# Kernel tuning notes

Hardware: AMD Instinct MI355X
Metric: run time of the kernel (lower is better)

## Reference

```python
import jax, jax.numpy as jnp
import numpy as np

MAX_AGENTS = 64
IN_DIM = 256
HID_DIM = 512
OUT_DIM = 256
MAX_CHILDREN = 8
BATCH = 1024


def setup_inputs() -> dict:
    key = jax.random.key(0)
    k1, k2, k3, k4, k5 = jax.random.split(key, 5)
    W1 = jax.random.normal(k1, (MAX_AGENTS, IN_DIM, HID_DIM), dtype=jnp.float32) * 0.02
    b1 = jnp.zeros((MAX_AGENTS, HID_DIM), dtype=jnp.float32)
    W2 = jax.random.normal(k2, (MAX_AGENTS, HID_DIM, OUT_DIM), dtype=jnp.float32) * 0.02
    b2 = jnp.zeros((MAX_AGENTS, OUT_DIM), dtype=jnp.float32)
    router_weights = jax.random.normal(k3, (MAX_AGENTS, HID_DIM, MAX_CHILDREN), dtype=jnp.float32) * 0.01
    agent_indices = jax.random.randint(k4, (BATCH,), 0, MAX_AGENTS, dtype=jnp.int64 if jax.config.jax_enable_x64 else jnp.int32)
    x = jax.random.normal(k5, (BATCH, IN_DIM), dtype=jnp.float32)
    return {
        "x": x,
        "W1": W1,
        "b1": b1,
        "W2": W2,
        "b2": b2,
        "router_weights": router_weights,
        "agent_indices": agent_indices,
    }


def reference(x, W1, b1, W2, b2, router_weights, agent_indices):
    # Gather per-sample weights (same as torch advanced indexing W1[agent_indices])
    w1 = W1[agent_indices]           # [B, In, Hid]
    b1g = b1[agent_indices]          # [B, Hid]
    w2 = W2[agent_indices]           # [B, Hid, Out]
    b2g = b2[agent_indices]          # [B, Out]
    rw = router_weights[agent_indices]  # [B, Hid, C]

    # per-sample MLP: bmm with a singleton row -> einsum
    h = jax.nn.relu(jnp.einsum('bi,bih->bh', x, w1) + b1g)      # [B, Hid]
    out = jnp.einsum('bh,bho->bo', h, w2) + b2g                 # [B, Out]
    r_logits = jnp.einsum('bh,bhc->bc', h, rw)                  # [B, C]
    return (h, out, r_logits)
```

## Files before the change

kernel.cpp:

```cpp
#include <hip/hip_runtime.h>

#define IN_DIM   256
#define HID_DIM  512
#define OUT_DIM  256
#define N_CHILD  8
#define BATCH    1024

#define SB    16
#define XPAD  20
#define MAXCH 128

__device__ __forceinline__ int sort_chunk(const int* __restrict__ raw, const int c,
                                          int* s_cnt, int* s_info, int* s_wsum,
                                          int* s_sid)
{
    const int t = threadIdx.x;
    const int lane = t & 63, w = t >> 6;
    if (t < 64) s_cnt[t] = 0;
    if (t == 0) { s_info[2] = 0; s_info[3] = 0; }
    __syncthreads();
    if (raw[2 * t + 1] != 0 || raw[2 * (t + 256) + 1] != 0) s_info[3] = 1;
    __syncthreads();
    const int is32 = s_info[3];
    int myid[4];
    #pragma unroll
    for (int j = 0; j < 4; ++j) {
        const int i = t * 4 + j;
        const int v = (is32 ? raw[i] : raw[2 * i]) & 63;
        myid[j] = v;
        atomicAdd(&s_cnt[v], 1);
    }
    __syncthreads();
    if (t < 64) {
        const int ca  = s_cnt[t];
        const int nch = (ca + SB - 1) / SB;
        int sn = nch;
        #pragma unroll
        for (int d = 1; d < 64; d <<= 1) {
            const int v = __shfl_up(sn, d);
            if (lane >= d) sn += v;
        }
        const int chb = sn - nch;
        if (c >= chb && c < chb + nch) {
            s_info[0] = t;
            const int p = (c - chb) * SB;
            s_info[1] = p;
            s_info[2] = (ca - p < SB) ? (ca - p) : SB;
        }
    }
    __syncthreads();
    const int len = s_info[2];
    if (len == 0) return 0;
    const int a = s_info[0], p = s_info[1];
    int m = 0;
    #pragma unroll
    for (int j = 0; j < 4; ++j) if (myid[j] == a) ++m;
    int inc = m;
    #pragma unroll
    for (int d = 1; d < 64; d <<= 1) {
        const int v = __shfl_up(inc, d);
        if (lane >= d) inc += v;
    }
    if (lane == 63) s_wsum[w] = inc;
    __syncthreads();
    int base = inc - m;
    #pragma unroll
    for (int ww = 0; ww < 4; ++ww) if (ww < w) base += s_wsum[ww];
    #pragma unroll
    for (int j = 0; j < 4; ++j)
        if (myid[j] == a) {
            const int r = (base++) - p;
            if (r >= 0 && r < SB) s_sid[r] = t * 4 + j;
        }
    __syncthreads();
    if (t >= len && t < SB) s_sid[t] = s_sid[len - 1];
    __syncthreads();
    return len;
}

extern "C" __global__ __launch_bounds__(256)
void k1_mlp1(const float* __restrict__ x, const float* __restrict__ W1,
             const float* __restrict__ b1, const float* __restrict__ rw,
             const int* __restrict__ raw,
             float* __restrict__ h_out, float* __restrict__ r_part)
{
    __shared__ float xT[IN_DIM * XPAD];
    __shared__ float wS[64 * 64];
    __shared__ int s_cnt[64], s_info[4], s_wsum[4], s_sid[SB];

    const int chunk = blockIdx.x;
    const int t = threadIdx.x;
    const int len = sort_chunk(raw, chunk, s_cnt, s_info, s_wsum, s_sid);
    if (len == 0) return;
    const int a    = s_info[0];
    const int bcol = blockIdx.y * 64;

    const float* Wb = W1 + (size_t)a * IN_DIM * HID_DIM + bcol;
    const int sr  = t >> 4;
    const int sc4 = (t & 15) * 4;
    #define WLD(P,I) (*(const float4*)(Wb + (size_t)((P)*64 + sr + (I)*16) * HID_DIM + sc4))

    float4 wr0 = WLD(0,0), wr1 = WLD(0,1), wr2 = WLD(0,2), wr3 = WLD(0,3);

    #pragma unroll
    for (int s = 0; s < SB; ++s)
        xT[t * XPAD + s] = x[(size_t)s_sid[s] * IN_DIM + t];

    const int cg = t & 15;
    const int kq = (t >> 4) & 3;
    const int w  = t >> 6;
    const bool act = (w * 4) < len;

    float acc[16];
    #pragma unroll
    for (int i = 0; i < 16; ++i) acc[i] = 0.f;

    for (int p = 0; p < IN_DIM / 64; ++p) {
        __syncthreads();
        *(float4*)(&wS[(sr +  0) * 64 + sc4]) = wr0;
        *(float4*)(&wS[(sr + 16) * 64 + sc4]) = wr1;
        *(float4*)(&wS[(sr + 32) * 64 + sc4]) = wr2;
        *(float4*)(&wS[(sr + 48) * 64 + sc4]) = wr3;
        __syncthreads();
        if (p < 3) {
            wr0 = WLD(p+1,0); wr1 = WLD(p+1,1);
            wr2 = WLD(p+1,2); wr3 = WLD(p+1,3);
        }
        if (act) {
            #pragma unroll
            for (int i = 0; i < 16; ++i) {
                const int row = i * 4 + kq;
                const float4 wv = *(const float4*)(&wS[row * 64 + cg * 4]);
                const float4 xv = *(const float4*)(&xT[(p * 64 + row) * XPAD + w * 4]);
                const float wa[4] = {wv.x, wv.y, wv.z, wv.w};
                const float xa[4] = {xv.x, xv.y, xv.z, xv.w};
                #pragma unroll
                for (int c = 0; c < 4; ++c)
                    #pragma unroll
                    for (int s = 0; s < 4; ++s)
                        acc[c * 4 + s] = fmaf(wa[c], xa[s], acc[c * 4 + s]);
            }
        }
    }
    #undef WLD

    if (!act) return;
    #pragma unroll
    for (int i = 0; i < 16; ++i) {
        acc[i] += __shfl_xor(acc[i], 16);
        acc[i] += __shfl_xor(acc[i], 32);
    }
    if (kq != 0) return;

    const float4 bv = *(const float4*)(b1 + a * HID_DIM + bcol + cg * 4);
    const float ba[4] = {bv.x, bv.y, bv.z, bv.w};
    float hv[16];
    #pragma unroll
    for (int c = 0; c < 4; ++c)
        #pragma unroll
        for (int s = 0; s < 4; ++s)
            hv[c * 4 + s] = fmaxf(acc[c * 4 + s] + ba[c], 0.f);

    #pragma unroll
    for (int s = 0; s < 4; ++s) {
        float4 v = make_float4(hv[0 * 4 + s], hv[1 * 4 + s],
                               hv[2 * 4 + s], hv[3 * 4 + s]);
        *(float4*)(h_out + (size_t)s_sid[w * 4 + s] * HID_DIM + bcol + cg * 4) = v;
    }

    float rp[32];
    #pragma unroll
    for (int i = 0; i < 32; ++i) rp[i] = 0.f;
    const float* rwa = rw + (size_t)a * HID_DIM * N_CHILD
                          + (size_t)(bcol + cg * 4) * N_CHILD;
    #pragma unroll
    for (int j = 0; j < 4; ++j)
        #pragma unroll
        for (int ch = 0; ch < 8; ++ch) {
            const float rv = rwa[j * N_CHILD + ch];
            #pragma unroll
            for (int s = 0; s < 4; ++s)
                rp[s * 8 + ch] = fmaf(hv[j * 4 + s], rv, rp[s * 8 + ch]);
        }
    #pragma unroll
    for (int i = 0; i < 32; ++i) {
        rp[i] += __shfl_xor(rp[i], 1);
        rp[i] += __shfl_xor(rp[i], 2);
        rp[i] += __shfl_xor(rp[i], 4);
        rp[i] += __shfl_xor(rp[i], 8);
    }
    if (cg == 0) {
        float* rb = r_part + ((size_t)chunk * 8 + blockIdx.y) * 128 + w * 32;
        #pragma unroll
        for (int s4 = 0; s4 < 8; ++s4)
            *(float4*)(rb + s4 * 4) = make_float4(rp[s4*4+0], rp[s4*4+1],
                                                  rp[s4*4+2], rp[s4*4+3]);
    }
}

extern "C" __global__ __launch_bounds__(256)
void k2_mlp2(const float* __restrict__ h, const float* __restrict__ W2,
             const float* __restrict__ b2, const int* __restrict__ raw,
             const float* __restrict__ r_part,
             float* __restrict__ o_out, float* __restrict__ r_out)
{
    __shared__ float hT[64 * XPAD];
    __shared__ float wS[64 * 32];
    __shared__ int s_cnt[64], s_info[4], s_wsum[4], s_sid[SB];

    const int chunk = blockIdx.x;
    const int t = threadIdx.x;
    const int len = sort_chunk(raw, chunk, s_cnt, s_info, s_wsum, s_sid);
    if (len == 0) return;
    const int a    = s_info[0];
    const int bcol = blockIdx.y * 32;

    const float* Wb = W2 + (size_t)a * HID_DIM * OUT_DIM + bcol;
    const int r2   = t >> 3;
    const int c4   = (t & 7) * 4;
    const int hrow = t & 63;
    const int hsb  = (t >> 6) * 4;
    #define WLD2(P,I) (*(const float4*)(Wb + (size_t)((P)*64 + r2 + (I)*32) * OUT_DIM + c4))
    #define HLD(P,J)  (h[(size_t)s_sid[hsb + (J)] * HID_DIM + (P)*64 + hrow])

    float4 wr0 = WLD2(0,0), wr1 = WLD2(0,1);
    float  hr0 = HLD(0,0), hr1 = HLD(0,1), hr2 = HLD(0,2), hr3 = HLD(0,3);

    const int cg = t & 7;
    const int kq = (t >> 3) & 7;
    const int w  = t >> 6;
    const bool act = (w * 4) < len;

    float acc[16];
    #pragma unroll
    for (int i = 0; i < 16; ++i) acc[i] = 0.f;

    for (int p = 0; p < HID_DIM / 64; ++p) {
        __syncthreads();
        hT[hrow * XPAD + hsb + 0] = hr0;
        hT[hrow * XPAD + hsb + 1] = hr1;
        hT[hrow * XPAD + hsb + 2] = hr2;
        hT[hrow * XPAD + hsb + 3] = hr3;
        *(float4*)(&wS[(r2 +  0) * 32 + c4]) = wr0;
        *(float4*)(&wS[(r2 + 32) * 32 + c4]) = wr1;
        __syncthreads();
        if (p < 7) {
            wr0 = WLD2(p+1,0); wr1 = WLD2(p+1,1);
            hr0 = HLD(p+1,0);  hr1 = HLD(p+1,1);
            hr2 = HLD(p+1,2);  hr3 = HLD(p+1,3);
        }
        if (act) {
            #pragma unroll
            for (int i = 0; i < 8; ++i) {
                const int row = i * 8 + kq;
                const float4 wv = *(const float4*)(&wS[row * 32 + cg * 4]);
                const float4 xv = *(const float4*)(&hT[row * XPAD + w * 4]);
                const float wa[4] = {wv.x, wv.y, wv.z, wv.w};
                const float xa[4] = {xv.x, xv.y, xv.z, xv.w};
                #pragma unroll
                for (int c = 0; c < 4; ++c)
                    #pragma unroll
                    for (int s = 0; s < 4; ++s)
                        acc[c * 4 + s] = fmaf(wa[c], xa[s], acc[c * 4 + s]);
            }
        }
    }
    #undef WLD2
    #undef HLD

    #pragma unroll
    for (int i = 0; i < 16; ++i) {
        acc[i] += __shfl_xor(acc[i], 8);
        acc[i] += __shfl_xor(acc[i], 16);
        acc[i] += __shfl_xor(acc[i], 32);
    }
    if (act && kq == 0) {
        const float4 bv = *(const float4*)(b2 + a * OUT_DIM + bcol + cg * 4);
        #pragma unroll
        for (int s = 0; s < 4; ++s) {
            const int g = w * 4 + s;
            if (g < len) {
                float4 v = make_float4(acc[0 * 4 + s] + bv.x,
                                       acc[1 * 4 + s] + bv.y,
                                       acc[2 * 4 + s] + bv.z,
                                       acc[3 * 4 + s] + bv.w);
                *(float4*)(o_out + (size_t)s_sid[g] * OUT_DIM + bcol + cg * 4) = v;
            }
        }
    }
    if (blockIdx.y == 0 && t < 128) {
        const int s = t >> 3;
        if (s < len) {
            float sum = 0.f;
            #pragma unroll
            for (int yy = 0; yy < 8; ++yy)
                sum += r_part[((size_t)chunk * 8 + yy) * 128 + t];
            r_out[(size_t)s_sid[s] * N_CHILD + (t & 7)] = sum;
        }
    }
}

extern "C" void kernel_launch(void* const* d_in, const int* in_sizes, int n_in,
                              void* d_out, int out_size, void* d_ws, size_t ws_size,
                              hipStream_t stream) {
    const float* x  = (const float*)d_in[0];
    const float* W1 = (const float*)d_in[1];
    const float* b1 = (const float*)d_in[2];
    const float* W2 = (const float*)d_in[3];
    const float* b2 = (const float*)d_in[4];
    const float* rw = (const float*)d_in[5];
    const int* raw  = (const int*)d_in[6];

    float* r_part = (float*)d_ws;

    float* out   = (float*)d_out;
    float* h_out = out;
    float* o_out = h_out + (size_t)BATCH * HID_DIM;
    float* r_out = o_out + (size_t)BATCH * OUT_DIM;

    hipLaunchKernelGGL(k1_mlp1, dim3(MAXCH, 8), dim3(256), 0, stream,
                       x, W1, b1, rw, raw, h_out, r_part);
    hipLaunchKernelGGL(k2_mlp2, dim3(MAXCH, 8), dim3(256), 0, stream,
                       h_out, W2, b2, raw, r_part, o_out, r_out);
}
```

Measured before the change: 129.2 us.

## Fuse both MLP stages into one cooperative kernel with grid sync and swizzled LDS

Merges the two per-agent GEMM kernels into a single cooperative launch that does a grid-wide sync between the hidden-layer and output-layer phases, so the per-chunk agent sort and the second kernel launch happen only once. Each thread now computes 8 columns instead of 4, and the weight tile in shared memory uses an XOR swizzle to avoid bank conflicts. Stage 2 now runs on only 4 of the 8 y-blocks with 64-wide tiles, and a fifth y-block does the router reduction. A grid sync across 1024 blocks is required, and if the cooperative launch fails the code falls back to two launches.

Result: slower. 477.3 us (+269.5%).

```diff
diff --git a/kernel.cpp b/kernel.cpp
--- a/kernel.cpp
+++ b/kernel.cpp
@@ -1,4 +1,7 @@
 #include <hip/hip_runtime.h>
+#include <hip/hip_cooperative_groups.h>
+
+namespace cg = cooperative_groups;
 
 #define IN_DIM   256
 #define HID_DIM  512
@@ -78,224 +81,230 @@
     return len;
 }
 
-extern "C" __global__ __launch_bounds__(256)
-void k1_mlp1(const float* __restrict__ x, const float* __restrict__ W1,
-             const float* __restrict__ b1, const float* __restrict__ rw,
-             const int* __restrict__ raw,
-             float* __restrict__ h_out, float* __restrict__ r_part)
+extern "C" __global__ __launch_bounds__(256, 4)
+void fused(const float* __restrict__ x, const float* __restrict__ W1,
+           const float* __restrict__ b1, const float* __restrict__ W2,
+           const float* __restrict__ b2, const float* __restrict__ rw,
+           const int* __restrict__ raw, float* __restrict__ h_out,
+           float* __restrict__ r_part, float* __restrict__ o_out,
+           float* __restrict__ r_out, int mode)
 {
-    __shared__ float xT[IN_DIM * XPAD];
+    __shared__ float sm[IN_DIM * XPAD];
     __shared__ float wS[64 * 64];
     __shared__ int s_cnt[64], s_info[4], s_wsum[4], s_sid[SB];
 
-    const int chunk = blockIdx.x;
+    const int c = blockIdx.x;
     const int t = threadIdx.x;
-    const int len = sort_chunk(raw, chunk, s_cnt, s_info, s_wsum, s_sid);
-    if (len == 0) return;
-    const int a    = s_info[0];
-    const int bcol = blockIdx.y * 64;
-
-    const float* Wb = W1 + (size_t)a * IN_DIM * HID_DIM + bcol;
-    const int sr  = t >> 4;
-    const int sc4 = (t & 15) * 4;
-    #define WLD(P,I) (*(const float4*)(Wb + (size_t)((P)*64 + sr + (I)*16) * HID_DIM + sc4))
-
-    float4 wr0 = WLD(0,0), wr1 = WLD(0,1), wr2 = WLD(0,2), wr3 = WLD(0,3);
-
-    #pragma unroll
-    for (int s = 0; s < SB; ++s)
-        xT[t * XPAD + s] = x[(size_t)s_sid[s] * IN_DIM + t];
-
-    const int cg = t & 15;
-    const int kq = (t >> 4) & 3;
-    const int w  = t >> 6;
-    const bool act = (w * 4) < len;
-
-    float acc[16];
-    #pragma unroll
-    for (int i = 0; i < 16; ++i) acc[i] = 0.f;
-
-    for (int p = 0; p < IN_DIM / 64; ++p) {
-        __syncthreads();
-        *(float4*)(&wS[(sr +  0) * 64 + sc4]) = wr0;
-        *(float4*)(&wS[(sr + 16) * 64 + sc4]) = wr1;
-        *(float4*)(&wS[(sr + 32) * 64 + sc4]) = wr2;
-        *(float4*)(&wS[(sr + 48) * 64 + sc4]) = wr3;
-        __syncthreads();
-        if (p < 3) {
-            wr0 = WLD(p+1,0); wr1 = WLD(p+1,1);
-            wr2 = WLD(p+1,2); wr3 = WLD(p+1,3);
-        }
-        if (act) {
-            #pragma unroll
-            for (int i = 0; i < 16; ++i) {
-                const int row = i * 4 + kq;
-                const float4 wv = *(const float4*)(&wS[row * 64 + cg * 4]);
-                const float4 xv = *(const float4*)(&xT[(p * 64 + row) * XPAD + w * 4]);
-                const float wa[4] = {wv.x, wv.y, wv.z, wv.w};
-                const float xa[4] = {xv.x, xv.y, xv.z, xv.w};
-                #pragma unroll
-                for (int c = 0; c < 4; ++c)
-                    #pragma unroll
-                    for (int s = 0; s < 4; ++s)
-                        acc[c * 4 + s] = fmaf(wa[c], xa[s], acc[c * 4 + s]);
-            }
-        }
-    }
-    #undef WLD
-
-    if (!act) return;
-    #pragma unroll
-    for (int i = 0; i < 16; ++i) {
-        acc[i] += __shfl_xor(acc[i], 16);
-        acc[i] += __shfl_xor(acc[i], 32);
-    }
-    if (kq != 0) return;
-
-    const float4 bv = *(const float4*)(b1 + a * HID_DIM + bcol + cg * 4);
-    const float ba[4] = {bv.x, bv.y, bv.z, bv.w};
-    float hv[16];
-    #pragma unroll
-    for (int c = 0; c < 4; ++c)
-        #pragma unroll
-        for (int s = 0; s < 4; ++s)
-            hv[c * 4 + s] = fmaxf(acc[c * 4 + s] + ba[c], 0.f);
-
-    #pragma unroll
-    for (int s = 0; s < 4; ++s) {
-        float4 v = make_float4(hv[0 * 4 + s], hv[1 * 4 + s],
-                               hv[2 * 4 + s], hv[3 * 4 + s]);
-        *(float4*)(h_out + (size_t)s_sid[w * 4 + s] * HID_DIM + bcol + cg * 4) = v;
-    }
-
-    float rp[32];
-    #pragma unroll
-    for (int i = 0; i < 32; ++i) rp[i] = 0.f;
-    const float* rwa = rw + (size_t)a * HID_DIM * N_CHILD
-                          + (size_t)(bcol + cg * 4) * N_CHILD;
-    #pragma unroll
-    for (int j = 0; j < 4; ++j)
-        #pragma unroll
-        for (int ch = 0; ch < 8; ++ch) {
-            const float rv = rwa[j * N_CHILD + ch];
-            #pragma unroll
-            for (int s = 0; s < 4; ++s)
-                rp[s * 8 + ch] = fmaf(hv[j * 4 + s], rv, rp[s * 8 + ch]);
-        }
-    #pragma unroll
-    for (int i = 0; i < 32; ++i) {
-        rp[i] += __shfl_xor(rp[i], 1);
-        rp[i] += __shfl_xor(rp[i], 2);
-        rp[i] += __shfl_xor(rp[i], 4);
-        rp[i] += __shfl_xor(rp[i], 8);
-    }
-    if (cg == 0) {
-        float* rb = r_part + ((size_t)chunk * 8 + blockIdx.y) * 128 + w * 32;
-        #pragma unroll
-        for (int s4 = 0; s4 < 8; ++s4)
-            *(float4*)(rb + s4 * 4) = make_float4(rp[s4*4+0], rp[s4*4+1],
-                                                  rp[s4*4+2], rp[s4*4+3]);
-    }
-}
-
-extern "C" __global__ __launch_bounds__(256)
-void k2_mlp2(const float* __restrict__ h, const float* __restrict__ W2,
-             const float* __restrict__ b2, const int* __restrict__ raw,
-             const float* __restrict__ r_part,
-             float* __restrict__ o_out, float* __restrict__ r_out)
-{
-    __shared__ float hT[64 * XPAD];
-    __shared__ float wS[64 * 32];
-    __shared__ int s_cnt[64], s_info[4], s_wsum[4], s_sid[SB];
-
-    const int chunk = blockIdx.x;
-    const int t = threadIdx.x;
-    const int len = sort_chunk(raw, chunk, s_cnt, s_info, s_wsum, s_sid);
-    if (len == 0) return;
-    const int a    = s_info[0];
-    const int bcol = blockIdx.y * 32;
-
-    const float* Wb = W2 + (size_t)a * HID_DIM * OUT_DIM + bcol;
-    const int r2   = t >> 3;
-    const int c4   = (t & 7) * 4;
-    const int hrow = t & 63;
-    const int hsb  = (t >> 6) * 4;
-    #define WLD2(P,I) (*(const float4*)(Wb + (size_t)((P)*64 + r2 + (I)*32) * OUT_DIM + c4))
-    #define HLD(P,J)  (h[(size_t)s_sid[hsb + (J)] * HID_DIM + (P)*64 + hrow])
-
-    float4 wr0 = WLD2(0,0), wr1 = WLD2(0,1);
-    float  hr0 = HLD(0,0), hr1 = HLD(0,1), hr2 = HLD(0,2), hr3 = HLD(0,3);
+    const int len = sort_chunk(raw, c, s_cnt, s_info, s_wsum, s_sid);
+    const int a   = s_info[0];
 
     const int cg = t & 7;
     const int kq = (t >> 3) & 7;
     const int w  = t >> 6;
     const bool act = (w * 4) < len;
-
-    float acc[16];
-    #pragma unroll
-    for (int i = 0; i < 16; ++i) acc[i] = 0.f;
-
-    for (int p = 0; p < HID_DIM / 64; ++p) {
-        __syncthreads();
-        hT[hrow * XPAD + hsb + 0] = hr0;
-        hT[hrow * XPAD + hsb + 1] = hr1;
-        hT[hrow * XPAD + hsb + 2] = hr2;
-        hT[hrow * XPAD + hsb + 3] = hr3;
-        *(float4*)(&wS[(r2 +  0) * 32 + c4]) = wr0;
-        *(float4*)(&wS[(r2 + 32) * 32 + c4]) = wr1;
-        __syncthreads();
-        if (p < 7) {
-            wr0 = WLD2(p+1,0); wr1 = WLD2(p+1,1);
-            hr0 = HLD(p+1,0);  hr1 = HLD(p+1,1);
-            hr2 = HLD(p+1,2);  hr3 = HLD(p+1,3);
-        }
+    const int sr  = t >> 4;
+    const int gc4 = (t & 15) * 4;
+    const int slt = ((t & 15) ^ sr) * 4;
+
+    if (mode != 2 && len > 0) {
+        const int bcol = blockIdx.y * 64;
+        const float* Wb = W1 + (size_t)a * IN_DIM * HID_DIM + bcol;
+        #define WLD(P,I) (*(const float4*)(Wb + (size_t)((P)*64 + sr + (I)*16) * HID_DIM + gc4))
+
+        float4 wr0 = WLD(0,0), wr1 = WLD(0,1), wr2 = WLD(0,2), wr3 = WLD(0,3);
+
+        #pragma unroll
+        for (int s = 0; s < SB; ++s)
+            sm[t * XPAD + s] = x[(size_t)s_sid[s] * IN_DIM + t];
+
+        float acc[32];
+        #pragma unroll
+        for (int i = 0; i < 32; ++i) acc[i] = 0.f;
+
+        for (int p = 0; p < IN_DIM / 64; ++p) {
+            __syncthreads();
+            *(float4*)(&wS[(sr +  0) * 64 + slt]) = wr0;
+            *(float4*)(&wS[(sr + 16) * 64 + slt]) = wr1;
+            *(float4*)(&wS[(sr + 32) * 64 + slt]) = wr2;
+            *(float4*)(&wS[(sr + 48) * 64 + slt]) = wr3;
+            __syncthreads();
+            if (p < 3) {
+                wr0 = WLD(p+1,0); wr1 = WLD(p+1,1);
+                wr2 = WLD(p+1,2); wr3 = WLD(p+1,3);
+            }
+            if (act) {
+                #pragma unroll
+                for (int i = 0; i < 8; ++i) {
+                    const int row = i * 8 + kq;
+                    const int rs  = row & 15;
+                    const float4 wv0 = *(const float4*)(&wS[row * 64 + ((2*cg    ^ rs) * 4)]);
+                    const float4 wv1 = *(const float4*)(&wS[row * 64 + (((2*cg+1) ^ rs) * 4)]);
+                    const float4 xv  = *(const float4*)(&sm[(p * 64 + row) * XPAD + w * 4]);
+                    const float wa[8] = {wv0.x, wv0.y, wv0.z, wv0.w,
+                                         wv1.x, wv1.y, wv1.z, wv1.w};
+                    const float xa[4] = {xv.x, xv.y, xv.z, xv.w};
+                    #pragma unroll
+                    for (int cc = 0; cc < 8; ++cc)
+                        #pragma unroll
+                        for (int s = 0; s < 4; ++s)
+                            acc[cc * 4 + s] = fmaf(wa[cc], xa[s], acc[cc * 4 + s]);
+                }
+            }
+        }
+        #undef WLD
+
         if (act) {
             #pragma unroll
-            for (int i = 0; i < 8; ++i) {
-                const int row = i * 8 + kq;
-                const float4 wv = *(const float4*)(&wS[row * 32 + cg * 4]);
-                const float4 xv = *(const float4*)(&hT[row * XPAD + w * 4]);
-                const float wa[4] = {wv.x, wv.y, wv.z, wv.w};
-                const float xa[4] = {xv.x, xv.y, xv.z, xv.w};
-                #pragma unroll
-                for (int c = 0; c < 4; ++c)
+            for (int i = 0; i < 32; ++i) {
+                acc[i] += __shfl_xor(acc[i], 8);
+                acc[i] += __shfl_xor(acc[i], 16);
+                acc[i] += __shfl_xor(acc[i], 32);
+            }
+            if (kq == 0) {
+                const float4 bv0 = *(const float4*)(b1 + a * HID_DIM + bcol + cg * 8);
+                const float4 bv1 = *(const float4*)(b1 + a * HID_DIM + bcol + cg * 8 + 4);
+                const float ba[8] = {bv0.x, bv0.y, bv0.z, bv0.w,
+                                     bv1.x, bv1.y, bv1.z, bv1.w};
+                float hv[32];
+                #pragma unroll
+                for (int cc = 0; cc < 8; ++cc)
                     #pragma unroll
                     for (int s = 0; s < 4; ++s)
-                        acc[c * 4 + s] = fmaf(wa[c], xa[s], acc[c * 4 + s]);
-            }
-        }
-    }
-    #undef WLD2
-    #undef HLD
-
-    #pragma unroll
-    for (int i = 0; i < 16; ++i) {
-        acc[i] += __shfl_xor(acc[i], 8);
-        acc[i] += __shfl_xor(acc[i], 16);
-        acc[i] += __shfl_xor(acc[i], 32);
-    }
-    if (act && kq == 0) {
-        const float4 bv = *(const float4*)(b2 + a * OUT_DIM + bcol + cg * 4);
-        #pragma unroll
-        for (int s = 0; s < 4; ++s) {
-            const int g = w * 4 + s;
-            if (g < len) {
-                float4 v = make_float4(acc[0 * 4 + s] + bv.x,
-                                       acc[1 * 4 + s] + bv.y,
-                                       acc[2 * 4 + s] + bv.z,
-                                       acc[3 * 4 + s] + bv.w);
-                *(float4*)(o_out + (size_t)s_sid[g] * OUT_DIM + bcol + cg * 4) = v;
-            }
-        }
-    }
-    if (blockIdx.y == 0 && t < 128) {
-        const int s = t >> 3;
-        if (s < len) {
-            float sum = 0.f;
+                        hv[cc * 4 + s] = fmaxf(acc[cc * 4 + s] + ba[cc], 0.f);
+
+                #pragma unroll
+                for (int s = 0; s < 4; ++s) {
+                    float* hb = h_out + (size_t)s_sid[w * 4 + s] * HID_DIM + bcol + cg * 8;
+                    *(float4*)(hb)     = make_float4(hv[0*4+s], hv[1*4+s], hv[2*4+s], hv[3*4+s]);
+                    *(float4*)(hb + 4) = make_float4(hv[4*4+s], hv[5*4+s], hv[6*4+s], hv[7*4+s]);
+                }
+
+                float rp[32];
+                #pragma unroll
+                for (int i = 0; i < 32; ++i) rp[i] = 0.f;
+                const float* rwa = rw + (size_t)a * HID_DIM * N_CHILD
+                                      + (size_t)(bcol + cg * 8) * N_CHILD;
+                #pragma unroll
+                for (int j = 0; j < 8; ++j)
+                    #pragma unroll
+                    for (int ch = 0; ch < 8; ++ch) {
+                        const float rv = rwa[j * N_CHILD + ch];
+                        #pragma unroll
+                        for (int s = 0; s < 4; ++s)
+                            rp[s * 8 + ch] = fmaf(hv[j * 4 + s], rv, rp[s * 8 + ch]);
+                    }
+                #pragma unroll
+                for (int i = 0; i < 32; ++i) {
+                    rp[i] += __shfl_xor(rp[i], 1);
+                    rp[i] += __shfl_xor(rp[i], 2);
+                    rp[i] += __shfl_xor(rp[i], 4);
+                }
+                if (cg == 0) {
+                    float* rb = r_part + ((size_t)c * 8 + blockIdx.y) * 128 + w * 32;
+                    #pragma unroll
+                    for (int s4 = 0; s4 < 8; ++s4)
+                        *(float4*)(rb + s4 * 4) = make_float4(rp[s4*4+0], rp[s4*4+1],
+                                                              rp[s4*4+2], rp[s4*4+3]);
+                }
+            }
+        }
+    }
+
+    if (mode == 0) {
+        __threadfence();
+        cg::this_grid().sync();
+        __threadfence();
+    }
+
+    if (mode != 1 && len > 0) {
+        if (blockIdx.y < 4) {
+            const int bcol = blockIdx.y * 64;
+            const float* Wb = W2 + (size_t)a * HID_DIM * OUT_DIM + bcol;
+            const int hrow = t & 63;
+            const int hsb  = (t >> 6) * 4;
+            #define WLD2(P,I) (*(const float4*)(Wb + (size_t)((P)*64 + sr + (I)*16) * OUT_DIM + gc4))
+            #define HLD(P,J)  (h_out[(size_t)s_sid[hsb + (J)] * HID_DIM + (P)*64 + hrow])
+
+            float4 wr0 = WLD2(0,0), wr1 = WLD2(0,1), wr2 = WLD2(0,2), wr3 = WLD2(0,3);
+            float  hr0 = HLD(0,0),  hr1 = HLD(0,1),  hr2 = HLD(0,2),  hr3 = HLD(0,3);
+
+            float acc[32];
             #pragma unroll
-            for (int yy = 0; yy < 8; ++yy)
-                sum += r_part[((size_t)chunk * 8 + yy) * 128 + t];
-            r_out[(size_t)s_sid[s] * N_CHILD + (t & 7)] = sum;
+            for (int i = 0; i < 32; ++i) acc[i] = 0.f;
+
+            for (int p = 0; p < HID_DIM / 64; ++p) {
+                __syncthreads();
+                sm[hrow * XPAD + hsb + 0] = hr0;
+                sm[hrow * XPAD + hsb + 1] = hr1;
+                sm[hrow * XPAD + hsb + 2] = hr2;
+                sm[hrow * XPAD + hsb + 3] = hr3;
+                *(float4*)(&wS[(sr +  0) * 64 + slt]) = wr0;
+                *(float4*)(&wS[(sr + 16) * 64 + slt]) = wr1;
+                *(float4*)(&wS[(sr + 32) * 64 + slt]) = wr2;
+                *(float4*)(&wS[(sr + 48) * 64 + slt]) = wr3;
+                __syncthreads();
+                if (p < 7) {
+                    wr0 = WLD2(p+1,0); wr1 = WLD2(p+1,1);
+                    wr2 = WLD2(p+1,2); wr3 = WLD2(p+1,3);
+                    hr0 = HLD(p+1,0);  hr1 = HLD(p+1,1);
+                    hr2 = HLD(p+1,2);  hr3 = HLD(p+1,3);
+                }
+                if (act) {
+                    #pragma unroll
+                    for (int i = 0; i < 8; ++i) {
+                        const int row = i * 8 + kq;
+                        const int rs  = row & 15;
+                        const float4 wv0 = *(const float4*)(&wS[row * 64 + ((2*cg    ^ rs) * 4)]);
+                        const float4 wv1 = *(const float4*)(&wS[row * 64 + (((2*cg+1) ^ rs) * 4)]);
+                        const float4 xv  = *(const float4*)(&sm[row * XPAD + w * 4]);
+                        const float wa[8] = {wv0.x, wv0.y, wv0.z, wv0.w,
+                                             wv1.x, wv1.y, wv1.z, wv1.w};
+                        const float xa[4] = {xv.x, xv.y, xv.z, xv.w};
+                        #pragma unroll
+                        for (int cc = 0; cc < 8; ++cc)
+                            #pragma unroll
+                            for (int s = 0; s < 4; ++s)
+                                acc[cc * 4 + s] = fmaf(wa[cc], xa[s], acc[cc * 4 + s]);
+                    }
+                }
+            }
+            #undef WLD2
+            #undef HLD
+
+            if (act) {
+                #pragma unroll
+                for (int i = 0; i < 32; ++i) {
+                    acc[i] += __shfl_xor(acc[i], 8);
+                    acc[i] += __shfl_xor(acc[i], 16);
+                    acc[i] += __shfl_xor(acc[i], 32);
+                }
+                if (kq == 0) {
+                    const float4 bv0 = *(const float4*)(b2 + a * OUT_DIM + bcol + cg * 8);
+                    const float4 bv1 = *(const float4*)(b2 + a * OUT_DIM + bcol + cg * 8 + 4);
+                    #pragma unroll
+                    for (int s = 0; s < 4; ++s) {
+                        const int g = w * 4 + s;
+                        if (g < len) {
+                            float* op = o_out + (size_t)s_sid[g] * OUT_DIM + bcol + cg * 8;
+                            *(float4*)(op)     = make_float4(acc[0*4+s] + bv0.x, acc[1*4+s] + bv0.y,
+                                                             acc[2*4+s] + bv0.z, acc[3*4+s] + bv0.w);
+                            *(float4*)(op + 4) = make_float4(acc[4*4+s] + bv1.x, acc[5*4+s] + bv1.y,
+                                                             acc[6*4+s] + bv1.z, acc[7*4+s] + bv1.w);
+                        }
+                    }
+                }
+            }
+        } else if (blockIdx.y == 4) {
+            if (t < 128) {
+                const int s = t >> 3;
+                if (s < len) {
+                    float sum = 0.f;
+                    #pragma unroll
+                    for (int yy = 0; yy < 8; ++yy)
+                        sum += r_part[((size_t)c * 8 + yy) * 128 + t];
+                    r_out[(size_t)s_sid[s] * N_CHILD + (t & 7)] = sum;
+                }
+            }
         }
     }
 }
@@ -318,8 +327,19 @@
     float* o_out = h_out + (size_t)BATCH * HID_DIM;
     float* r_out = o_out + (size_t)BATCH * OUT_DIM;
 
-    hipLaunchKernelGGL(k1_mlp1, dim3(MAXCH, 8), dim3(256), 0, stream,
-                       x, W1, b1, rw, raw, h_out, r_part);
-    hipLaunchKernelGGL(k2_mlp2, dim3(MAXCH, 8), dim3(256), 0, stream,
-                       h_out, W2, b2, raw, r_part, o_out, r_out);
+    int mode = 0;
+    void* args[] = {(void*)&x, (void*)&W1, (void*)&b1, (void*)&W2, (void*)&b2,
+                    (void*)&rw, (void*)&raw, (void*)&h_out, (void*)&r_part,
+                    (void*)&o_out, (void*)&r_out, (void*)&mode};
+    hipError_t e = hipLaunchCooperativeKernel((const void*)fused, dim3(MAXCH, 8),
+                                              dim3(256), args, 0, stream);
+    if (e != hipSuccess) {
+        (void)hipGetLastError();
+        hipLaunchKernelGGL(fused, dim3(MAXCH, 8), dim3(256), 0, stream,
+                           x, W1, b1, W2, b2, rw, raw, h_out, r_part,
+                           o_out, r_out, 1);
+        hipLaunchKernelGGL(fused, dim3(MAXCH, 8), dim3(256), 0, stream,
+                           x, W1, b1, W2, b2, rw, raw, h_out, r_part,
+                           o_out, r_out, 2);
+    }
 }
```

## Read weights directly from global memory instead of staging through LDS tiles

Applied to the files above, without the earlier changes.

Both MLP kernels stop cooperatively staging weight tiles into shared memory with register double-buffering. Each thread now reads its float4 weight slice straight from global memory inside a fully unrolled k loop, relying on L1/L2 for the reuse across waves. This removes the per-tile barriers and the LDS traffic. k2 now stages h in two 256-row halves, and both kernels request 4 blocks per CU via launch bounds. The cost is that all four waves in a block read the same weight addresses redundantly from cache, and register pressure rises from the deep unroll.

New measurement: 145.1 us. +12.4%, slower.

```diff
diff --git a/kernel.cpp b/kernel.cpp
--- a/kernel.cpp
+++ b/kernel.cpp
@@ -78,73 +78,52 @@
     return len;
 }
 
-extern "C" __global__ __launch_bounds__(256)
+extern "C" __global__ __launch_bounds__(256, 4)
 void k1_mlp1(const float* __restrict__ x, const float* __restrict__ W1,
              const float* __restrict__ b1, const float* __restrict__ rw,
              const int* __restrict__ raw,
              float* __restrict__ h_out, float* __restrict__ r_part)
 {
     __shared__ float xT[IN_DIM * XPAD];
-    __shared__ float wS[64 * 64];
     __shared__ int s_cnt[64], s_info[4], s_wsum[4], s_sid[SB];
 
-    const int chunk = blockIdx.x;
+    const int c = blockIdx.x;
     const int t = threadIdx.x;
-    const int len = sort_chunk(raw, chunk, s_cnt, s_info, s_wsum, s_sid);
+    const int len = sort_chunk(raw, c, s_cnt, s_info, s_wsum, s_sid);
     if (len == 0) return;
-    const int a    = s_info[0];
+    const int a = s_info[0];
     const int bcol = blockIdx.y * 64;
-
-    const float* Wb = W1 + (size_t)a * IN_DIM * HID_DIM + bcol;
-    const int sr  = t >> 4;
-    const int sc4 = (t & 15) * 4;
-    #define WLD(P,I) (*(const float4*)(Wb + (size_t)((P)*64 + sr + (I)*16) * HID_DIM + sc4))
-
-    float4 wr0 = WLD(0,0), wr1 = WLD(0,1), wr2 = WLD(0,2), wr3 = WLD(0,3);
 
     #pragma unroll
     for (int s = 0; s < SB; ++s)
         xT[t * XPAD + s] = x[(size_t)s_sid[s] * IN_DIM + t];
+    __syncthreads();
 
     const int cg = t & 15;
     const int kq = (t >> 4) & 3;
     const int w  = t >> 6;
-    const bool act = (w * 4) < len;
+    if (w * 4 >= len) return;
+
+    const float* Wb = W1 + (size_t)a * IN_DIM * HID_DIM + bcol + cg * 4;
 
     float acc[16];
     #pragma unroll
     for (int i = 0; i < 16; ++i) acc[i] = 0.f;
 
-    for (int p = 0; p < IN_DIM / 64; ++p) {
-        __syncthreads();
-        *(float4*)(&wS[(sr +  0) * 64 + sc4]) = wr0;
-        *(float4*)(&wS[(sr + 16) * 64 + sc4]) = wr1;
-        *(float4*)(&wS[(sr + 32) * 64 + sc4]) = wr2;
-        *(float4*)(&wS[(sr + 48) * 64 + sc4]) = wr3;
-        __syncthreads();
-        if (p < 3) {
-            wr0 = WLD(p+1,0); wr1 = WLD(p+1,1);
-            wr2 = WLD(p+1,2); wr3 = WLD(p+1,3);
-        }
-        if (act) {
-            #pragma unroll
-            for (int i = 0; i < 16; ++i) {
-                const int row = i * 4 + kq;
-                const float4 wv = *(const float4*)(&wS[row * 64 + cg * 4]);
-                const float4 xv = *(const float4*)(&xT[(p * 64 + row) * XPAD + w * 4]);
-                const float wa[4] = {wv.x, wv.y, wv.z, wv.w};
-                const float xa[4] = {xv.x, xv.y, xv.z, xv.w};
-                #pragma unroll
-                for (int c = 0; c < 4; ++c)
-                    #pragma unroll
-                    for (int s = 0; s < 4; ++s)
-                        acc[c * 4 + s] = fmaf(wa[c], xa[s], acc[c * 4 + s]);
-            }
-        }
-    }
-    #undef WLD
-
-    if (!act) return;
+    #pragma unroll
+    for (int i = 0; i < 64; ++i) {
+        const int row = i * 4 + kq;
+        const float4 wv = *(const float4*)(Wb + (size_t)row * HID_DIM);
+        const float4 xv = *(const float4*)(&xT[row * XPAD + w * 4]);
+        const float wa[4] = {wv.x, wv.y, wv.z, wv.w};
+        const float xa[4] = {xv.x, xv.y, xv.z, xv.w};
+        #pragma unroll
+        for (int cc = 0; cc < 4; ++cc)
+            #pragma unroll
+            for (int s = 0; s < 4; ++s)
+                acc[cc * 4 + s] = fmaf(wa[cc], xa[s], acc[cc * 4 + s]);
+    }
+
     #pragma unroll
     for (int i = 0; i < 16; ++i) {
         acc[i] += __shfl_xor(acc[i], 16);
@@ -156,10 +135,10 @@
     const float ba[4] = {bv.x, bv.y, bv.z, bv.w};
     float hv[16];
     #pragma unroll
-    for (int c = 0; c < 4; ++c)
+    for (int cc = 0; cc < 4; ++cc)
         #pragma unroll
         for (int s = 0; s < 4; ++s)
-            hv[c * 4 + s] = fmaxf(acc[c * 4 + s] + ba[c], 0.f);
+            hv[cc * 4 + s] = fmaxf(acc[cc * 4 + s] + ba[cc], 0.f);
 
     #pragma unroll
     for (int s = 0; s < 4; ++s) {
@@ -190,7 +169,7 @@
         rp[i] += __shfl_xor(rp[i], 8);
     }
     if (cg == 0) {
-        float* rb = r_part + ((size_t)chunk * 8 + blockIdx.y) * 128 + w * 32;
+        float* rb = r_part + ((size_t)c * 8 + blockIdx.y) * 128 + w * 32;
         #pragma unroll
         for (int s4 = 0; s4 < 8; ++s4)
             *(float4*)(rb + s4 * 4) = make_float4(rp[s4*4+0], rp[s4*4+1],
@@ -198,93 +177,74 @@
     }
 }
 
-extern "C" __global__ __launch_bounds__(256)
+extern "C" __global__ __launch_bounds__(256, 4)
 void k2_mlp2(const float* __restrict__ h, const float* __restrict__ W2,
              const float* __restrict__ b2, const int* __restrict__ raw,
              const float* __restrict__ r_part,
              float* __restrict__ o_out, float* __restrict__ r_out)
 {
-    __shared__ float hT[64 * XPAD];
-    __shared__ float wS[64 * 32];
+    __shared__ float hT[256 * XPAD];
     __shared__ int s_cnt[64], s_info[4], s_wsum[4], s_sid[SB];
 
-    const int chunk = blockIdx.x;
+    const int c = blockIdx.x;
     const int t = threadIdx.x;
-    const int len = sort_chunk(raw, chunk, s_cnt, s_info, s_wsum, s_sid);
+    const int len = sort_chunk(raw, c, s_cnt, s_info, s_wsum, s_sid);
     if (len == 0) return;
-    const int a    = s_info[0];
+    const int a = s_info[0];
     const int bcol = blockIdx.y * 32;
-
-    const float* Wb = W2 + (size_t)a * HID_DIM * OUT_DIM + bcol;
-    const int r2   = t >> 3;
-    const int c4   = (t & 7) * 4;
-    const int hrow = t & 63;
-    const int hsb  = (t >> 6) * 4;
-    #define WLD2(P,I) (*(const float4*)(Wb + (size_t)((P)*64 + r2 + (I)*32) * OUT_DIM + c4))
-    #define HLD(P,J)  (h[(size_t)s_sid[hsb + (J)] * HID_DIM + (P)*64 + hrow])
-
-    float4 wr0 = WLD2(0,0), wr1 = WLD2(0,1);
-    float  hr0 = HLD(0,0), hr1 = HLD(0,1), hr2 = HLD(0,2), hr3 = HLD(0,3);
 
     const int cg = t & 7;
     const int kq = (t >> 3) & 7;
     const int w  = t >> 6;
     const bool act = (w * 4) < len;
+    const float* Wb = W2 + (size_t)a * HID_DIM * OUT_DIM + bcol + cg * 4;
 
     float acc[16];
     #pragma unroll
     for (int i = 0; i < 16; ++i) acc[i] = 0.f;
 
-    for (int p = 0; p < HID_DIM / 64; ++p) {
+    #pragma unroll
+    for (int half = 0; half < 2; ++half) {
+        const int kb = half * 256;
+        #pragma unroll
+        for (int s = 0; s < SB; ++s)
+            hT[t * XPAD + s] = h[(size_t)s_sid[s] * HID_DIM + kb + t];
         __syncthreads();
-        hT[hrow * XPAD + hsb + 0] = hr0;
-        hT[hrow * XPAD + hsb + 1] = hr1;
-        hT[hrow * XPAD + hsb + 2] = hr2;
-        hT[hrow * XPAD + hsb + 3] = hr3;
-        *(float4*)(&wS[(r2 +  0) * 32 + c4]) = wr0;
-        *(float4*)(&wS[(r2 + 32) * 32 + c4]) = wr1;
-        __syncthreads();
-        if (p < 7) {
-            wr0 = WLD2(p+1,0); wr1 = WLD2(p+1,1);
-            hr0 = HLD(p+1,0);  hr1 = HLD(p+1,1);
-            hr2 = HLD(p+1,2);  hr3 = HLD(p+1,3);
-        }
         if (act) {
             #pragma unroll
-            for (int i = 0; i < 8; ++i) {
+            for (int i = 0; i < 32; ++i) {
                 const int row = i * 8 + kq;
-                const float4 wv = *(const float4*)(&wS[row * 32 + cg * 4]);
+                const float4 wv = *(const float4*)(Wb + (size_t)(kb + row) * OUT_DIM);
                 const float4 xv = *(const float4*)(&hT[row * XPAD + w * 4]);
                 const float wa[4] = {wv.x, wv.y, wv.z, wv.w};
                 const float xa[4] = {xv.x, xv.y, xv.z, xv.w};
                 #pragma unroll
-                for (int c = 0; c < 4; ++c)
+                for (int cc = 0; cc < 4; ++cc)
                     #pragma unroll
                     for (int s = 0; s < 4; ++s)
-                        acc[c * 4 + s] = fmaf(wa[c], xa[s], acc[c * 4 + s]);
+                        acc[cc * 4 + s] = fmaf(wa[cc], xa[s], acc[cc * 4 + s]);
             }
         }
-    }
-    #undef WLD2
-    #undef HLD
-
-    #pragma unroll
-    for (int i = 0; i < 16; ++i) {
-        acc[i] += __shfl_xor(acc[i], 8);
-        acc[i] += __shfl_xor(acc[i], 16);
-        acc[i] += __shfl_xor(acc[i], 32);
-    }
-    if (act && kq == 0) {
-        const float4 bv = *(const float4*)(b2 + a * OUT_DIM + bcol + cg * 4);
-        #pragma unroll
-        for (int s = 0; s < 4; ++s) {
-            const int g = w * 4 + s;
-            if (g < len) {
-                float4 v = make_float4(acc[0 * 4 + s] + bv.x,
-                                       acc[1 * 4 + s] + bv.y,
-                                       acc[2 * 4 + s] + bv.z,
-                                       acc[3 * 4 + s] + bv.w);
-                *(float4*)(o_out + (size_t)s_sid[g] * OUT_DIM + bcol + cg * 4) = v;
+        if (half == 0) __syncthreads();
+    }
+
+    if (act) {
+        #pragma unroll
+        for (int i = 0; i < 16; ++i) {
+            acc[i] += __shfl_xor(acc[i], 8);
+            acc[i] += __shfl_xor(acc[i], 16);
+            acc[i] += __shfl_xor(acc[i], 32);
+        }
+        if (kq == 0) {
+            const float4 bv = *(const float4*)(b2 + a * OUT_DIM + bcol + cg * 4);
+            #pragma unroll
+            for (int s = 0; s < 4; ++s) {
+                const int g = w * 4 + s;
+                if (g < len) {
+                    float4 v = make_float4(acc[0*4+s] + bv.x, acc[1*4+s] + bv.y,
+                                           acc[2*4+s] + bv.z, acc[3*4+s] + bv.w);
+                    *(float4*)(o_out + (size_t)s_sid[g] * OUT_DIM + bcol + cg * 4) = v;
+                }
             }
         }
     }
@@ -294,7 +254,7 @@
             float sum = 0.f;
             #pragma unroll
             for (int yy = 0; yy < 8; ++yy)
-                sum += r_part[((size_t)chunk * 8 + yy) * 128 + t];
+                sum += r_part[((size_t)c * 8 + yy) * 128 + t];
             r_out[(size_t)s_sid[s] * N_CHILD + (t & 7)] = sum;
         }
     }
```

## Double per-block sample chunk and move router logits into second kernel

Applied to the files above, without the earlier changes.

Grows the per-agent chunk from 16 to 32 samples, so each weight tile is reused across twice as many samples and fewer chunks (96 max) are launched. The x tile is staged in two halves to keep shared memory small. The router logit computation moves from the first kernel's epilogue, which used partial sums and a workspace reduction, into the second kernel. There, blockIdx.y==0 blocks accumulate h·rw directly from the shared h tile. This removes the r_part round trip but doubles accumulator registers and adds serial router work to one column of blocks.

Measured after the change: 128.1 us. No clear change (-0.8%).

```diff
diff --git a/kernel.cpp b/kernel.cpp
--- a/kernel.cpp
+++ b/kernel.cpp
@@ -6,9 +6,9 @@
 #define N_CHILD  8
 #define BATCH    1024
 
-#define SB    16
-#define XPAD  20
-#define MAXCH 128
+#define SB    32
+#define XS    36
+#define MAXCH 96
 
 __device__ __forceinline__ int sort_chunk(const int* __restrict__ raw, const int c,
                                           int* s_cnt, int* s_info, int* s_wsum,
@@ -80,19 +80,18 @@
 
 extern "C" __global__ __launch_bounds__(256)
 void k1_mlp1(const float* __restrict__ x, const float* __restrict__ W1,
-             const float* __restrict__ b1, const float* __restrict__ rw,
-             const int* __restrict__ raw,
-             float* __restrict__ h_out, float* __restrict__ r_part)
+             const float* __restrict__ b1, const int* __restrict__ raw,
+             float* __restrict__ h_out)
 {
-    __shared__ float xT[IN_DIM * XPAD];
+    __shared__ float xT[128 * XS];
     __shared__ float wS[64 * 64];
     __shared__ int s_cnt[64], s_info[4], s_wsum[4], s_sid[SB];
 
-    const int chunk = blockIdx.x;
+    const int c = blockIdx.x;
     const int t = threadIdx.x;
-    const int len = sort_chunk(raw, chunk, s_cnt, s_info, s_wsum, s_sid);
+    const int len = sort_chunk(raw, c, s_cnt, s_info, s_wsum, s_sid);
     if (len == 0) return;
-    const int a    = s_info[0];
+    const int a = s_info[0];
     const int bcol = blockIdx.y * 64;
 
     const float* Wb = W1 + (size_t)a * IN_DIM * HID_DIM + bcol;
@@ -102,26 +101,39 @@
 
     float4 wr0 = WLD(0,0), wr1 = WLD(0,1), wr2 = WLD(0,2), wr3 = WLD(0,3);
 
-    #pragma unroll
-    for (int s = 0; s < SB; ++s)
-        xT[t * XPAD + s] = x[(size_t)s_sid[s] * IN_DIM + t];
+    const int xrow = t & 127;
+    const int xsg  = (t >> 7) * 16;
+    #pragma unroll
+    for (int j = 0; j < 16; ++j)
+        xT[xrow * XS + xsg + j] = x[(size_t)s_sid[xsg + j] * IN_DIM + xrow];
 
     const int cg = t & 15;
     const int kq = (t >> 4) & 3;
     const int w  = t >> 6;
-    const bool act = (w * 4) < len;
-
-    float acc[16];
-    #pragma unroll
-    for (int i = 0; i < 16; ++i) acc[i] = 0.f;
-
-    for (int p = 0; p < IN_DIM / 64; ++p) {
+    const bool act = (w * 8) < len;
+
+    float acc[32];
+    #pragma unroll
+    for (int i = 0; i < 32; ++i) acc[i] = 0.f;
+    float xh[16];
+
+    for (int p = 0; p < 4; ++p) {
         __syncthreads();
+        if (p == 2) {
+            #pragma unroll
+            for (int j = 0; j < 16; ++j)
+                xT[xrow * XS + xsg + j] = xh[j];
+        }
         *(float4*)(&wS[(sr +  0) * 64 + sc4]) = wr0;
         *(float4*)(&wS[(sr + 16) * 64 + sc4]) = wr1;
         *(float4*)(&wS[(sr + 32) * 64 + sc4]) = wr2;
         *(float4*)(&wS[(sr + 48) * 64 + sc4]) = wr3;
         __syncthreads();
+        if (p == 1) {
+            #pragma unroll
+            for (int j = 0; j < 16; ++j)
+                xh[j] = x[(size_t)s_sid[xsg + j] * IN_DIM + 128 + xrow];
+        }
         if (p < 3) {
             wr0 = WLD(p+1,0); wr1 = WLD(p+1,1);
             wr2 = WLD(p+1,2); wr3 = WLD(p+1,3);
@@ -130,15 +142,18 @@
             #pragma unroll
             for (int i = 0; i < 16; ++i) {
                 const int row = i * 4 + kq;
-                const float4 wv = *(const float4*)(&wS[row * 64 + cg * 4]);
-                const float4 xv = *(const float4*)(&xT[(p * 64 + row) * XPAD + w * 4]);
+                const int lr  = (p & 1) * 64 + row;
+                const float4 wv  = *(const float4*)(&wS[row * 64 + cg * 4]);
+                const float4 xv0 = *(const float4*)(&xT[lr * XS + w * 8]);
+                const float4 xv1 = *(const float4*)(&xT[lr * XS + w * 8 + 4]);
                 const float wa[4] = {wv.x, wv.y, wv.z, wv.w};
-                const float xa[4] = {xv.x, xv.y, xv.z, xv.w};
+                const float xa[8] = {xv0.x, xv0.y, xv0.z, xv0.w,
+                                     xv1.x, xv1.y, xv1.z, xv1.w};
                 #pragma unroll
-                for (int c = 0; c < 4; ++c)
+                for (int cc = 0; cc < 4; ++cc)
                     #pragma unroll
-                    for (int s = 0; s < 4; ++s)
-                        acc[c * 4 + s] = fmaf(wa[c], xa[s], acc[c * 4 + s]);
+                    for (int s = 0; s < 8; ++s)
+                        acc[cc * 8 + s] = fmaf(wa[cc], xa[s], acc[cc * 8 + s]);
             }
         }
     }
@@ -146,130 +161,120 @@
 
     if (!act) return;
     #pragma unroll
-    for (int i = 0; i < 16; ++i) {
+    for (int i = 0; i < 32; ++i) {
         acc[i] += __shfl_xor(acc[i], 16);
         acc[i] += __shfl_xor(acc[i], 32);
     }
     if (kq != 0) return;
 
     const float4 bv = *(const float4*)(b1 + a * HID_DIM + bcol + cg * 4);
-    const float ba[4] = {bv.x, bv.y, bv.z, bv.w};
-    float hv[16];
-    #pragma unroll
-    for (int c = 0; c < 4; ++c)
-        #pragma unroll
-        for (int s = 0; s < 4; ++s)
-            hv[c * 4 + s] = fmaxf(acc[c * 4 + s] + ba[c], 0.f);
-
-    #pragma unroll
-    for (int s = 0; s < 4; ++s) {
-        float4 v = make_float4(hv[0 * 4 + s], hv[1 * 4 + s],
-                               hv[2 * 4 + s], hv[3 * 4 + s]);
-        *(float4*)(h_out + (size_t)s_sid[w * 4 + s] * HID_DIM + bcol + cg * 4) = v;
-    }
-
-    float rp[32];
-    #pragma unroll
-    for (int i = 0; i < 32; ++i) rp[i] = 0.f;
-    const float* rwa = rw + (size_t)a * HID_DIM * N_CHILD
-                          + (size_t)(bcol + cg * 4) * N_CHILD;
-    #pragma unroll
-    for (int j = 0; j < 4; ++j)
-        #pragma unroll
-        for (int ch = 0; ch < 8; ++ch) {
-            const float rv = rwa[j * N_CHILD + ch];
-            #pragma unroll
-            for (int s = 0; s < 4; ++s)
-                rp[s * 8 + ch] = fmaf(hv[j * 4 + s], rv, rp[s * 8 + ch]);
-        }
-    #pragma unroll
-    for (int i = 0; i < 32; ++i) {
-        rp[i] += __shfl_xor(rp[i], 1);
-        rp[i] += __shfl_xor(rp[i], 2);
-        rp[i] += __shfl_xor(rp[i], 4);
-        rp[i] += __shfl_xor(rp[i], 8);
-    }
-    if (cg == 0) {
-        float* rb = r_part + ((size_t)chunk * 8 + blockIdx.y) * 128 + w * 32;
-        #pragma unroll
-        for (int s4 = 0; s4 < 8; ++s4)
-            *(float4*)(rb + s4 * 4) = make_float4(rp[s4*4+0], rp[s4*4+1],
-                                                  rp[s4*4+2], rp[s4*4+3]);
+    #pragma unroll
+    for (int s = 0; s < 8; ++s) {
+        float4 v = make_float4(fmaxf(acc[0*8+s] + bv.x, 0.f),
+                               fmaxf(acc[1*8+s] + bv.y, 0.f),
+                               fmaxf(acc[2*8+s] + bv.z, 0.f),
+                               fmaxf(acc[3*8+s] + bv.w, 0.f));
+        *(float4*)(h_out + (size_t)s_sid[w * 8 + s] * HID_DIM + bcol + cg * 4) = v;
     }
 }
 
 extern "C" __global__ __launch_bounds__(256)
 void k2_mlp2(const float* __restrict__ h, const float* __restrict__ W2,
-             const float* __restrict__ b2, const int* __restrict__ raw,
-             const float* __restrict__ r_part,
+             const float* __restrict__ b2, const float* __restrict__ rw,
+             const int* __restrict__ raw,
              float* __restrict__ o_out, float* __restrict__ r_out)
 {
-    __shared__ float hT[64 * XPAD];
+    __shared__ float hT[64 * XS];
     __shared__ float wS[64 * 32];
+    __shared__ float rwS[64 * N_CHILD];
     __shared__ int s_cnt[64], s_info[4], s_wsum[4], s_sid[SB];
 
-    const int chunk = blockIdx.x;
+    const int c = blockIdx.x;
     const int t = threadIdx.x;
-    const int len = sort_chunk(raw, chunk, s_cnt, s_info, s_wsum, s_sid);
+    const int len = sort_chunk(raw, c, s_cnt, s_info, s_wsum, s_sid);
     if (len == 0) return;
-    const int a    = s_info[0];
+    const int a = s_info[0];
     const int bcol = blockIdx.y * 32;
-
-    const float* Wb = W2 + (size_t)a * HID_DIM * OUT_DIM + bcol;
-    const int r2   = t >> 3;
+    const bool router = (blockIdx.y == 0);
+
+    const float* Wb  = W2 + (size_t)a * HID_DIM * OUT_DIM + bcol;
+    const float* rwp = rw + (size_t)a * HID_DIM * N_CHILD;
+    const int r2w  = t >> 3;
     const int c4   = (t & 7) * 4;
     const int hrow = t & 63;
-    const int hsb  = (t >> 6) * 4;
-    #define WLD2(P,I) (*(const float4*)(Wb + (size_t)((P)*64 + r2 + (I)*32) * OUT_DIM + c4))
-    #define HLD(P,J)  (h[(size_t)s_sid[hsb + (J)] * HID_DIM + (P)*64 + hrow])
-
-    float4 wr0 = WLD2(0,0), wr1 = WLD2(0,1);
-    float  hr0 = HLD(0,0), hr1 = HLD(0,1), hr2 = HLD(0,2), hr3 = HLD(0,3);
+    const int hsb  = (t >> 6) * 8;
+    #define WLD2(P,I) (*(const float4*)(Wb + (size_t)((P)*64 + r2w + (I)*32) * OUT_DIM + c4))
+
+    float4 wA0 = WLD2(0,0), wA1 = WLD2(0,1);
+    float hA[8], hB[8];
+    #pragma unroll
+    for (int j = 0; j < 8; ++j)
+        hA[j] = h[(size_t)s_sid[hsb + j] * HID_DIM + hrow];
+    float rA0 = 0.f, rA1 = 0.f;
+    if (router) { rA0 = rwp[t]; rA1 = rwp[256 + t]; }
 
     const int cg = t & 7;
     const int kq = (t >> 3) & 7;
     const int w  = t >> 6;
-    const bool act = (w * 4) < len;
-
-    float acc[16];
-    #pragma unroll
-    for (int i = 0; i < 16; ++i) acc[i] = 0.f;
-
-    for (int p = 0; p < HID_DIM / 64; ++p) {
+    const bool act = (w * 8) < len;
+    const int rs  = t >> 3;
+    const int rch = t & 7;
+
+    float acc[32];
+    #pragma unroll
+    for (int i = 0; i < 32; ++i) acc[i] = 0.f;
+    float racc = 0.f;
+
+    for (int p = 0; p < 8; ++p) {
         __syncthreads();
-        hT[hrow * XPAD + hsb + 0] = hr0;
-        hT[hrow * XPAD + hsb + 1] = hr1;
-        hT[hrow * XPAD + hsb + 2] = hr2;
-        hT[hrow * XPAD + hsb + 3] = hr3;
-        *(float4*)(&wS[(r2 +  0) * 32 + c4]) = wr0;
-        *(float4*)(&wS[(r2 + 32) * 32 + c4]) = wr1;
+        #pragma unroll
+        for (int j = 0; j < 8; ++j)
+            hT[hrow * XS + hsb + j] = hA[j];
+        *(float4*)(&wS[(r2w +  0) * 32 + c4]) = wA0;
+        *(float4*)(&wS[(r2w + 32) * 32 + c4]) = wA1;
+        if (router) { rwS[t] = rA0; rwS[256 + t] = rA1; }
         __syncthreads();
         if (p < 7) {
-            wr0 = WLD2(p+1,0); wr1 = WLD2(p+1,1);
-            hr0 = HLD(p+1,0);  hr1 = HLD(p+1,1);
-            hr2 = HLD(p+1,2);  hr3 = HLD(p+1,3);
+            wA0 = WLD2(p+1,0); wA1 = WLD2(p+1,1);
+            #pragma unroll
+            for (int j = 0; j < 8; ++j)
+                hB[j] = h[(size_t)s_sid[hsb + j] * HID_DIM + (p+1)*64 + hrow];
+            if (router) {
+                rA0 = rwp[(size_t)(p+1)*512 + t];
+                rA1 = rwp[(size_t)(p+1)*512 + 256 + t];
+            }
         }
         if (act) {
             #pragma unroll
             for (int i = 0; i < 8; ++i) {
                 const int row = i * 8 + kq;
-                const float4 wv = *(const float4*)(&wS[row * 32 + cg * 4]);
-                const float4 xv = *(const float4*)(&hT[row * XPAD + w * 4]);
+                const float4 wv  = *(const float4*)(&wS[row * 32 + cg * 4]);
+                const float4 xv0 = *(const float4*)(&hT[row * XS + w * 8]);
+                const float4 xv1 = *(const float4*)(&hT[row * XS + w * 8 + 4]);
                 const float wa[4] = {wv.x, wv.y, wv.z, wv.w};
-                const float xa[4] = {xv.x, xv.y, xv.z, xv.w};
+                const float xa[8] = {xv0.x, xv0.y, xv0.z, xv0.w,
+                                     xv1.x, xv1.y, xv1.z, xv1.w};
                 #pragma unroll
-                for (int c = 0; c < 4; ++c)
+                for (int cc = 0; cc < 4; ++cc)
                     #pragma unroll
-                    for (int s = 0; s < 4; ++s)
-                        acc[c * 4 + s] = fmaf(wa[c], xa[s], acc[c * 4 + s]);
+                    for (int s = 0; s < 8; ++s)
+                        acc[cc * 8 + s] = fmaf(wa[cc], xa[s], acc[cc * 8 + s]);
             }
         }
+        if (router) {
+            #pragma unroll
+            for (int row = 0; row < 64; ++row)
+                racc = fmaf(hT[row * XS + rs], rwS[row * N_CHILD + rch], racc);
+        }
+        if (p < 7) {
+            #pragma unroll
+            for (int j = 0; j < 8; ++j) hA[j] = hB[j];
+        }
     }
     #undef WLD2
-    #undef HLD
-
-    #pragma unroll
-    for (int i = 0; i < 16; ++i) {
+
+    #pragma unroll
+    for (int i = 0; i < 32; ++i) {
         acc[i] += __shfl_xor(acc[i], 8);
         acc[i] += __shfl_xor(acc[i], 16);
         acc[i] += __shfl_xor(acc[i], 32);
@@ -277,27 +282,17 @@
     if (act && kq == 0) {
         const float4 bv = *(const float4*)(b2 + a * OUT_DIM + bcol + cg * 4);
         #pragma unroll
-        for (int s = 0; s < 4; ++s) {
-            const int g = w * 4 + s;
+        for (int s = 0; s < 8; ++s) {
+            const int g = w * 8 + s;
             if (g < len) {
-                float4 v = make_float4(acc[0 * 4 + s] + bv.x,
-                                       acc[1 * 4 + s] + bv.y,
-                                       acc[2 * 4 + s] + bv.z,
-                                       acc[3 * 4 + s] + bv.w);
+                float4 v = make_float4(acc[0*8+s] + bv.x, acc[1*8+s] + bv.y,
+                                       acc[2*8+s] + bv.z, acc[3*8+s] + bv.w);
                 *(float4*)(o_out + (size_t)s_sid[g] * OUT_DIM + bcol + cg * 4) = v;
             }
         }
     }
-    if (blockIdx.y == 0 && t < 128) {
-        const int s = t >> 3;
-        if (s < len) {
-            float sum = 0.f;
-            #pragma unroll
-            for (int yy = 0; yy < 8; ++yy)
-                sum += r_part[((size_t)chunk * 8 + yy) * 128 + t];
-            r_out[(size_t)s_sid[s] * N_CHILD + (t & 7)] = sum;
-        }
-    }
+    if (router && rs < len)
+        r_out[(size_t)s_sid[rs] * N_CHILD + rch] = racc;
 }
 
 extern "C" void kernel_launch(void* const* d_in, const int* in_sizes, int n_in,
@@ -311,15 +306,13 @@
     const float* rw = (const float*)d_in[5];
     const int* raw  = (const int*)d_in[6];
 
-    float* r_part = (float*)d_ws;
-
     float* out   = (float*)d_out;
     float* h_out = out;
     float* o_out = h_out + (size_t)BATCH * HID_DIM;
     float* r_out = o_out + (size_t)BATCH * OUT_DIM;
 
     hipLaunchKernelGGL(k1_mlp1, dim3(MAXCH, 8), dim3(256), 0, stream,
-                       x, W1, b1, rw, raw, h_out, r_part);
+                       x, W1, b1, raw, h_out);
     hipLaunchKernelGGL(k2_mlp2, dim3(MAXCH, 8), dim3(256), 0, stream,
-                       h_out, W2, b2, raw, r_part, o_out, r_out);
+                       h_out, W2, b2, rw, raw, o_out, r_out);
 }
```
